# Kernel tuning notes

Hardware: AMD Instinct MI355X
Metric: run time of the kernel (lower is better)

## Reference

```python
import jax, jax.numpy as jnp
import numpy as np

B, NPG = 128, 512            # graphs, nodes per graph (batch is contiguous & uniform)
N = B * NPG                  # 65536 nodes
DEG = 8
E = N * DEG                  # 524288 edges
F_IN, NHID = 128, 64
H, C = 3, NHID               # GAT heads, out channels per head
HC = H * C                   # 192
NCLS = 10
RATIO = 0.5
NEG_SLOPE = 0.2


def setup_inputs() -> dict:
    key = jax.random.key(0)
    ks = jax.random.split(key, 24)
    x = jax.random.normal(ks[0], (N, F_IN), jnp.float32)
    # edges constrained within each graph (graphs are contiguous blocks of NPG nodes)
    offs = jnp.repeat(jnp.arange(B, dtype=jnp.int32) * NPG, NPG * DEG)
    src = jax.random.randint(ks[1], (E,), 0, NPG, dtype=jnp.int32) + offs
    dst = jax.random.randint(ks[2], (E,), 0, NPG, dtype=jnp.int32) + offs
    edge_index = jnp.stack([src, dst], axis=0)
    edge_attr = jax.random.normal(ks[3], (E, 2), jnp.float32)
    batch = jnp.repeat(jnp.arange(B, dtype=jnp.int32), NPG)

    def lin(k, o, i):
        return jax.random.normal(k, (o, i), jnp.float32) / np.float32(np.sqrt(i))

    return {
        "x": x, "edge_index": edge_index, "edge_attr": edge_attr, "batch": batch,
        # lin: num_features -> nhid//2
        "W_lin": lin(ks[4], NHID // 2, F_IN), "b_lin": jnp.zeros((NHID // 2,), jnp.float32),
        # GATConv(nhid//2 -> nhid, heads=3, edge_dim=2)
        "W_src": lin(ks[5], HC, NHID // 2),
        "att_src": jax.random.normal(ks[6], (H, C), jnp.float32) / np.float32(np.sqrt(C)),
        "att_dst": jax.random.normal(ks[7], (H, C), jnp.float32) / np.float32(np.sqrt(C)),
        "W_edge": lin(ks[8], HC, 2),
        "att_edge": jax.random.normal(ks[9], (H, C), jnp.float32) / np.float32(np.sqrt(C)),
        "b_gat": jnp.zeros((HC,), jnp.float32),
        # SAGPool score layer: GCNConv(nhid*3 -> 1)
        "W_gcn": lin(ks[10], 1, HC), "b_gcn": jnp.zeros((1,), jnp.float32),
        # classifier MLP
        "W1": lin(ks[11], NHID, 2 * HC), "b1": jnp.zeros((NHID,), jnp.float32),
        "W2": lin(ks[12], NHID // 2, NHID), "b2": jnp.zeros((NHID // 2,), jnp.float32),
        "W3": lin(ks[13], NCLS, NHID // 2), "b3": jnp.zeros((NCLS,), jnp.float32),
    }


def reference(x, edge_index, edge_attr, batch,
              W_lin, b_lin, W_src, att_src, att_dst, W_edge, att_edge, b_gat,
              W_gcn, b_gcn, W1, b1, W2, b2, W3, b3):
    src, dst = edge_index[0], edge_index[1]

    # ---- lin + ELU -------------------------------------------------------
    h = jax.nn.elu(x @ W_lin.T + b_lin)                       # [N, nhid//2]

    # ---- GATConv(heads=3, edge_dim=2), add_self_loops fill_value='mean' --
    loop = jnp.arange(N, dtype=src.dtype)
    cnt = jax.ops.segment_sum(jnp.ones((E,), h.dtype), dst, num_segments=N)
    loop_attr = jax.ops.segment_sum(edge_attr, dst, num_segments=N) / jnp.maximum(cnt, 1.0)[:, None]
    s_full = jnp.concatenate([src, loop])
    d_full = jnp.concatenate([dst, loop])
    ea_full = jnp.concatenate([edge_attr, loop_attr], axis=0)  # [E+N, 2]

    xp = (h @ W_src.T).reshape(N, H, C)                        # projected per-head feats
    a_src = (xp * att_src).sum(-1)                             # [N, H]
    a_dst = (xp * att_dst).sum(-1)                             # [N, H]
    ef = (ea_full @ W_edge.T).reshape(-1, H, C)
    a_edge = (ef * att_edge).sum(-1)                           # [E+N, H]

    alpha = jax.nn.leaky_relu(a_src[s_full] + a_dst[d_full] + a_edge, NEG_SLOPE)
    m = jax.ops.segment_max(alpha, d_full, num_segments=N)     # scatter-softmax over dst
    ealpha = jnp.exp(alpha - m[d_full])
    denom = jax.ops.segment_sum(ealpha, d_full, num_segments=N)
    alpha = ealpha / (denom[d_full] + 1e-16)                   # [E+N, H]

    out = jax.ops.segment_sum(alpha[:, :, None] * xp[s_full], d_full, num_segments=N)
    x1 = jax.nn.relu(out.reshape(N, HC) + b_gat)               # [N, 192]

    # ---- SAGPool: GCNConv score + per-graph top-k (mask form) ------------
    xw = x1 @ W_gcn.T                                          # [N, 1]
    deg = jax.ops.segment_sum(jnp.ones((E,), x1.dtype), dst, num_segments=N) + 1.0
    dinv = jax.lax.rsqrt(deg)
    agg = jax.ops.segment_sum((dinv[src] * dinv[dst])[:, None] * xw[src], dst, num_segments=N)
    score = (agg + (dinv ** 2)[:, None] * xw + b_gcn)[:, 0]    # [N]

    k = int(np.ceil(RATIO * NPG))                              # nodes kept per graph
    s2 = score.reshape(B, NPG)
    rank = jnp.argsort(jnp.argsort(-s2, axis=1), axis=1)
    mask = rank < k                                            # [B, NPG] top-k selection

    xs = (x1 * jnp.tanh(score)[:, None]).reshape(B, NPG, HC)
    gmp = jnp.max(jnp.where(mask[:, :, None], xs, -jnp.inf), axis=1)   # [B, 192]
    gap = jnp.sum(jnp.where(mask[:, :, None], xs, 0.0), axis=1) / k    # [B, 192]
    r = jnp.concatenate([gmp, gap], axis=1)                    # [B, 384]

    # ---- classifier MLP (dropout is identity in eval) ---------------------
    r = jax.nn.relu(r @ W1.T + b1)
    r = jax.nn.relu(r @ W2.T + b2)
    return jax.nn.log_softmax(r @ W3.T + b3, axis=-1)          # [B, num_classes]
```

## Files before the change

kernel.cpp:

```cpp
#include <hip/hip_runtime.h>
#include <hip/hip_bf16.h>
#include <math.h>

#define NN   65536
#define EE   524288
#define BB   128
#define NPGC 512
#define HCC  192
#define KSEL 256
#define NEG  0.2f
#define PSEG 16
#define SEGN (NPGC / PSEG)
#define MAXD 40
#define SLOTS ((size_t)NN * MAXD)
#define EPG   4096
#define HSTR  36

__device__ __forceinline__ int nodeblock_base(int bx) {
    int xcd = bx & 7, j = bx >> 3;
    int g = xcd + 8 * (j >> 1);
    return g * NPGC + (j & 1) * 256;
}

__global__ __launch_bounds__(192) void k_v(
    const float* __restrict__ W_src, const float* __restrict__ att_src,
    const float* __restrict__ att_dst, const float* __restrict__ W_edge,
    const float* __restrict__ att_edge, float* __restrict__ vbuf) {
    __shared__ float red[6];
    int t = threadIdx.x;
    if (t < 6) red[t] = 0.f;
    __syncthreads();
    {
        float ae = att_edge[t];
        int h = t >> 6;
        atomicAdd(&red[h],     W_edge[2 * t]     * ae);
        atomicAdd(&red[3 + h], W_edge[2 * t + 1] * ae);
    }
    if (t < 96) {
        int h = t >> 5, k = t & 31;
        float vs = 0.f, vd = 0.f;
        for (int c = 0; c < 64; ++c) {
            float w = W_src[(h * 64 + c) * 32 + k];
            vs += w * att_src[h * 64 + c];
            vd += w * att_dst[h * 64 + c];
        }
        vbuf[t] = vs;
        vbuf[96 + t] = vd;
    }
    __syncthreads();
    if (t < 6) vbuf[192 + t] = red[t];
}

__global__ __launch_bounds__(256) void k_feat(
    const float* __restrict__ x, const float* __restrict__ W_lin,
    const float* __restrict__ b_lin, const float* __restrict__ W_src,
    const float* __restrict__ vbuf,
    float* __restrict__ xp, float* __restrict__ ap_s, float* __restrict__ ap_d) {
    __shared__ float Wl[128 * HSTR];
    __shared__ float hs[128 * HSTR];
    __shared__ float vs_s[96], vd_s[96];
    int t = threadIdx.x;
    for (int i = t; i < 4096; i += 256) {
        int j = i >> 7, k = i & 127;
        Wl[k * HSTR + j] = W_lin[i];
    }
    if (t < 96) { vs_s[t] = vbuf[t]; vd_s[t] = vbuf[96 + t]; }
    __syncthreads();
    int bx = blockIdx.x;
    int xcd = bx & 7, j2 = bx >> 3;
    int g = xcd + 8 * (j2 >> 2);
    int nb = g * NPGC + (j2 & 3) * 128;
    int nl = t >> 1, hf = t & 1;
    int n = nb + nl;
    const float4* xr = (const float4*)(x + (size_t)n * 128);
    float acc[16];
#pragma unroll
    for (int j = 0; j < 16; ++j) acc[j] = b_lin[hf * 16 + j];
#pragma unroll 4
    for (int q = 0; q < 32; ++q) {
        float4 a = xr[q];
        const float* w = &Wl[(q * 4) * HSTR + hf * 16];
#pragma unroll
        for (int j = 0; j < 16; ++j) {
            acc[j] += a.x * w[j] + a.y * w[HSTR + j] +
                      a.z * w[2 * HSTR + j] + a.w * w[3 * HSTR + j];
        }
    }
#pragma unroll
    for (int j = 0; j < 16; ++j)
        acc[j] = acc[j] > 0.f ? acc[j] : expm1f(acc[j]);
#pragma unroll
    for (int head = 0; head < 3; ++head) {
        float s = 0.f, d = 0.f;
#pragma unroll
        for (int j = 0; j < 16; ++j) {
            s += acc[j] * vs_s[head * 32 + hf * 16 + j];
            d += acc[j] * vd_s[head * 32 + hf * 16 + j];
        }
        s += __shfl_xor(s, 1, 64);
        d += __shfl_xor(d, 1, 64);
        if (hf == 0) {
            ap_s[(size_t)head * NN + n] = s;
            ap_d[(size_t)head * NN + n] = d;
        }
    }
    float4* hw = (float4*)&hs[nl * HSTR + hf * 16];
#pragma unroll
    for (int q = 0; q < 4; ++q)
        hw[q] = make_float4(acc[4 * q], acc[4 * q + 1],
                            acc[4 * q + 2], acc[4 * q + 3]);
    __syncthreads();
    int lane = t & 63, wave = t >> 6;
    float wreg[96];
#pragma unroll
    for (int h = 0; h < 3; ++h) {
        const float4* wp = (const float4*)(W_src + (h * 64 + lane) * 32);
#pragma unroll
        for (int q = 0; q < 8; ++q) {
            float4 w = wp[q];
            wreg[h * 32 + 4 * q]     = w.x;
            wreg[h * 32 + 4 * q + 1] = w.y;
            wreg[h * 32 + 4 * q + 2] = w.z;
            wreg[h * 32 + 4 * q + 3] = w.w;
        }
    }
    int n0 = wave * 32;
    for (int nd = 0; nd < 32; ++nd) {
        int nl2 = n0 + nd;
        const float4* hr = (const float4*)&hs[nl2 * HSTR];
        float a0 = 0.f, a1 = 0.f, a2 = 0.f;
#pragma unroll
        for (int q = 0; q < 8; ++q) {
            float4 hv = hr[q];
            a0 += hv.x*wreg[4*q] + hv.y*wreg[4*q+1] + hv.z*wreg[4*q+2] + hv.w*wreg[4*q+3];
            a1 += hv.x*wreg[32+4*q] + hv.y*wreg[32+4*q+1] + hv.z*wreg[32+4*q+2] + hv.w*wreg[32+4*q+3];
            a2 += hv.x*wreg[64+4*q] + hv.y*wreg[64+4*q+1] + hv.z*wreg[64+4*q+2] + hv.w*wreg[64+4*q+3];
        }
        size_t nbase = (size_t)(nb + nl2) * HCC;
        xp[nbase + lane] = a0;
        xp[nbase + 64 + lane] = a1;
        xp[nbase + 128 + lane] = a2;
    }
}

__global__ __launch_bounds__(1024) void k_edges(
    const int* __restrict__ ei, const float* __restrict__ ea,
    const float* __restrict__ ap_s, const float* __restrict__ ap_d,
    const float* __restrict__ vbuf,
    int* __restrict__ fill, float4* __restrict__ slotA) {
    __shared__ int   s_pos[NPGC];
    __shared__ float s_la[NPGC * 2];
    __shared__ float s_as[NPGC * 3], s_ad[NPGC * 3];
    int b = blockIdx.x, t = threadIdx.x;
    int g = (b & 7) + 8 * (b >> 3);
    int nbase = g * NPGC;
    int ebase = g * EPG;
    if (t < NPGC) s_pos[t] = 0;
    s_la[t] = 0.f;
    for (int i = t; i < NPGC * 3; i += 1024) {
        int h = i >> 9, nl = i & (NPGC - 1);
        s_as[nl * 3 + h] = ap_s[(size_t)h * NN + nbase + nl];
        s_ad[nl * 3 + h] = ap_d[(size_t)h * NN + nbase + nl];
    }
    float ac[6];
#pragma unroll
    for (int h = 0; h < 6; ++h) ac[h] = vbuf[192 + h];
    int4  se  = ((const int4*)(ei + ebase))[t];
    int4  de  = ((const int4*)(ei + EE + ebase))[t];
    float4 a0 = ((const float4*)(ea + 2 * ebase))[2 * t];
    float4 a1 = ((const float4*)(ea + 2 * ebase))[2 * t + 1];
    __syncthreads();

    int   ss[4] = {se.x, se.y, se.z, se.w};
    int   dd[4] = {de.x, de.y, de.z, de.w};
    float e0v[4] = {a0.x, a0.z, a1.x, a1.z};
    float e1v[4] = {a0.y, a0.w, a1.y, a1.w};
#pragma unroll
    for (int k = 0; k < 4; ++k) {
        int s = ss[k], d = dd[k];
        int sl = s & (NPGC - 1), dl = d & (NPGC - 1);
        float e0 = e0v[k], e1 = e1v[k];
        atomicAdd(&s_la[2 * dl],     e0);
        atomicAdd(&s_la[2 * dl + 1], e1);
        float v[3];
#pragma unroll
        for (int h = 0; h < 3; ++h) {
            float a = s_as[sl * 3 + h] + s_ad[dl * 3 + h] +
                      e0 * ac[h] + e1 * ac[3 + h];
            v[h] = a >= 0.f ? a : NEG * a;
        }
        int pos = atomicAdd(&s_pos[dl], 1);
        if (pos < MAXD - 1)
            slotA[(size_t)(nbase + dl) * MAXD + 1 + pos] =
                make_float4(v[0], v[1], v[2], __int_as_float(s));
    }
    __syncthreads();
    if (t < NPGC) {
        int cnt = s_pos[t];
        int n = nbase + t;
        fill[n] = cnt;
        float inv = 1.f / fmaxf((float)cnt, 1.f);
        float l0 = s_la[2 * t] * inv, l1 = s_la[2 * t + 1] * inv;
        float v[3];
#pragma unroll
        for (int h = 0; h < 3; ++h) {
            float a = s_as[t * 3 + h] + s_ad[t * 3 + h] +
                      l0 * ac[h] + l1 * ac[3 + h];
            v[h] = a >= 0.f ? a : NEG * a;
        }
        slotA[(size_t)n * MAXD] = make_float4(v[0], v[1], v[2],
                                              __int_as_float(n));
    }
}

__global__ __launch_bounds__(256) void k_agg(
    const int* __restrict__ fill, const float4* __restrict__ slotA,
    const float* __restrict__ xp,
    const float* __restrict__ b_gat, const float* __restrict__ W_gcn,
    float* __restrict__ x1, float* __restrict__ xwd, float* __restrict__ dinv) {
    __shared__ float2 wsl[4][3][65];
    int wave = threadIdx.x >> 6, lane = threadIdx.x & 63;
    int b = blockIdx.x;
    int xcd = b & 7, j = b >> 3;
    int g = (j >> 7) * 8 + xcd;
    int n = g * NPGC + (j & 127) * 4 + wave;

    int ctrue = fill[n];
    int cnt = ctrue < (MAXD - 1) ? ctrue : (MAXD - 1);
    int tot = cnt + 1;

    if (lane < tot) {
        float4 pk = slotA[(size_t)n * MAXD + lane];
        wsl[wave][0][lane] = make_float2(__expf(pk.x), pk.w);
        wsl[wave][1][lane] = make_float2(__expf(pk.y), pk.w);
        wsl[wave][2][lane] = make_float2(__expf(pk.z), pk.w);
    }
    bool act = lane < 48;
    int head = act ? (lane >> 4) : 0;
    const float2* wp = &wsl[wave][head][0];
    const float4* xp4 = (const float4*)xp;
    float ax = 0.f, ay = 0.f, az = 0.f, aw = 0.f, den = 0.f;
    int s = 0;
    for (; s + 3 < tot; s += 4) {
        float2 wsA = wp[s],     wsB = wp[s + 1];
        float2 wsC = wp[s + 2], wsD = wp[s + 3];
        den += (wsA.x + wsB.x) + (wsC.x + wsD.x);
        if (act) {
            float4 vA = xp4[(size_t)__float_as_int(wsA.y) * 48 + lane];
            float4 vB = xp4[(size_t)__float_as_int(wsB.y) * 48 + lane];
            float4 vC = xp4[(size_t)__float_as_int(wsC.y) * 48 + lane];
            float4 vD = xp4[(size_t)__float_as_int(wsD.y) * 48 + lane];
            ax += wsA.x * vA.x + wsB.x * vB.x + wsC.x * vC.x + wsD.x * vD.x;
            ay += wsA.x * vA.y + wsB.x * vB.y + wsC.x * vC.y + wsD.x * vD.y;
            az += wsA.x * vA.z + wsB.x * vB.z + wsC.x * vC.z + wsD.x * vD.z;
            aw += wsA.x * vA.w + wsB.x * vB.w + wsC.x * vC.w + wsD.x * vD.w;
        }
    }
    for (; s < tot; ++s) {
        float2 wsA = wp[s];
        den += wsA.x;
        if (act) {
            float4 vA = xp4[(size_t)__float_as_int(wsA.y) * 48 + lane];
            ax += wsA.x * vA.x; ay += wsA.x * vA.y;
            az += wsA.x * vA.z; aw += wsA.x * vA.w;
        }
    }
    float p = 0.f;
    if (act) {
        float id = 1.f / (den + 1e-16f);
        float4 bg = ((const float4*)b_gat)[lane];
        float4 v;
        v.x = fmaxf(ax * id + bg.x, 0.f);
        v.y = fmaxf(ay * id + bg.y, 0.f);
        v.z = fmaxf(az * id + bg.z, 0.f);
        v.w = fmaxf(aw * id + bg.w, 0.f);
        ((float4*)x1)[(size_t)n * 48 + lane] = v;
        float4 wg = ((const float4*)W_gcn)[lane];
        p = v.x * wg.x + v.y * wg.y + v.z * wg.z + v.w * wg.w;
    }
#pragma unroll
    for (int msk = 32; msk > 0; msk >>= 1) p += __shfl_xor(p, msk, 64);
    if (lane == 0) {
        float dv = rsqrtf((float)ctrue + 1.f);
        xwd[n] = p * dv;
        dinv[n] = dv;
    }
}

__global__ __launch_bounds__(256) void k_score(
    const int* __restrict__ fill, const float4* __restrict__ slotA,
    const float* __restrict__ xwd, const float* __restrict__ dinv,
    const float* __restrict__ b_gcn, float* __restrict__ score) {
    int wave = threadIdx.x >> 6, lane = threadIdx.x & 63;
    int b = blockIdx.x;
    int xcd = b & 7, j = b >> 3;
    int g = (j >> 7) * 8 + xcd;
    int n = g * NPGC + (j & 127) * 4 + wave;

    int ctrue = fill[n];
    int cnt = ctrue < (MAXD - 1) ? ctrue : (MAXD - 1);
    float acc = 0.f;
    if (lane <= cnt) {
        int src = __float_as_int(
            ((const float*)slotA)[((size_t)n * MAXD + lane) * 4 + 3]);
        acc = xwd[src];
    }
#pragma unroll
    for (int msk = 32; msk > 0; msk >>= 1) acc += __shfl_xor(acc, msk, 64);
    if (lane == 0) score[n] = b_gcn[0] + dinv[n] * acc;
}

__global__ __launch_bounds__(192) void k_poolrank(
    const float* __restrict__ score, const float* __restrict__ x1,
    float* __restrict__ pmax, float* __restrict__ psum) {
    __shared__ float sc[NPGC];
    __shared__ float ts_s[SEGN];
    __shared__ int sel_s[SEGN];
    int b = blockIdx.x;
    int xcd = b & 7, gslot = (b >> 3) & 15, seg = b >> 7;
    int g = gslot * 8 + xcd;
    int t = threadIdx.x;
    int gbase = g * NPGC;
    for (int i = t; i < NPGC; i += 192) sc[i] = score[gbase + i];
    __syncthreads();
    if (t < SEGN) {
        int iloc = seg * SEGN + t;
        float si = sc[iloc];
        int rank = 0;
        for (int j = 0; j < NPGC; ++j) {
            float sj = sc[j];
            rank += (sj > si) || (sj == si && j < iloc);
        }
        sel_s[t] = (rank < KSEL) ? 1 : 0;
        ts_s[t] = tanhf(si);
    }
    __syncthreads();
    int nb = gbase + seg * SEGN;
    float mx = -1e30f, sm = 0.f;
    for (int i = 0; i < SEGN; ++i) {
        if (sel_s[i]) {
            float v = x1[(size_t)(nb + i) * HCC + t] * ts_s[i];
            mx = fmaxf(mx, v);
            sm += v;
        }
    }
    size_t pb = (size_t)(g * PSEG + seg) * HCC + t;
    pmax[pb] = mx;
    psum[pb] = sm;
}

__global__ __launch_bounds__(384) void k_mlp(
    const float* __restrict__ pmax, const float* __restrict__ psum,
    const float* __restrict__ W1, const float* __restrict__ b1,
    const float* __restrict__ W2, const float* __restrict__ b2,
    const float* __restrict__ W3, const float* __restrict__ b3,
    float* __restrict__ out) {
    __shared__ float rs[384], part[384], h1[64], h2[32], lg[10], mls;
    int g = blockIdx.x, t = threadIdx.x;
    if (t < HCC) {
        float mx = -1e30f, sm = 0.f;
#pragma unroll
        for (int s = 0; s < PSEG; ++s) {
            mx = fmaxf(mx, pmax[(size_t)(g * PSEG + s) * HCC + t]);
            sm += psum[(size_t)(g * PSEG + s) * HCC + t];
        }
        rs[t] = mx;
        rs[HCC + t] = sm * (1.f / (float)KSEL);
    }
    __syncthreads();
    {
        int o = t / 6, sl = t - o * 6;
        const float* wr = W1 + o * 384 + sl * 64;
        const float* rr = rs + sl * 64;
        float s = 0.f;
#pragma unroll 8
        for (int k = 0; k < 64; ++k) s += rr[k] * wr[k];
        part[t] = s;
    }
    __syncthreads();
    if (t < 64) {
        float s = b1[t];
#pragma unroll
        for (int j = 0; j < 6; ++j) s += part[t * 6 + j];
        h1[t] = fmaxf(s, 0.f);
    }
    __syncthreads();
    if (t < 256) {
        int o = t >> 3, sl = t & 7;
        const float* wr = W2 + o * 64 + sl * 8;
        const float* hr = h1 + sl * 8;
        float s = 0.f;
#pragma unroll
        for (int k = 0; k < 8; ++k) s += hr[k] * wr[k];
        part[t] = s;
    }
    __syncthreads();
    if (t < 32) {
        float s = b2[t];
#pragma unroll
        for (int j = 0; j < 8; ++j) s += part[t * 8 + j];
        h2[t] = fmaxf(s, 0.f);
    }
    __syncthreads();
    if (t < 10) {
        float s = b3[t];
        for (int k = 0; k < 32; ++k) s += h2[k] * W3[t * 32 + k];
        lg[t] = s;
    }
    __syncthreads();
    if (t == 0) {
        float mx = lg[0];
        for (int j = 1; j < 10; ++j) mx = fmaxf(mx, lg[j]);
        float se = 0.f;
        for (int j = 0; j < 10; ++j) se += expf(lg[j] - mx);
        mls = mx + logf(se);
    }
    __syncthreads();
    if (t < 10) out[g * 10 + t] = lg[t] - mls;
}

extern "C" void kernel_launch(void* const* d_in, const int* in_sizes, int n_in,
                              void* d_out, int out_size, void* d_ws, size_t ws_size,
                              hipStream_t stream) {
    const float* x        = (const float*)d_in[0];
    const int*   ei       = (const int*)d_in[1];
    const float* ea       = (const float*)d_in[2];
    const float* W_lin    = (const float*)d_in[4];
    const float* b_lin    = (const float*)d_in[5];
    const float* W_src    = (const float*)d_in[6];
    const float* att_src  = (const float*)d_in[7];
    const float* att_dst  = (const float*)d_in[8];
    const float* W_edge   = (const float*)d_in[9];
    const float* att_edge = (const float*)d_in[10];
    const float* b_gat    = (const float*)d_in[11];
    const float* W_gcn    = (const float*)d_in[12];
    const float* b_gcn    = (const float*)d_in[13];
    const float* W1 = (const float*)d_in[14]; const float* b1 = (const float*)d_in[15];
    const float* W2 = (const float*)d_in[16]; const float* b2 = (const float*)d_in[17];
    const float* W3 = (const float*)d_in[18]; const float* b3 = (const float*)d_in[19];
    float* out = (float*)d_out;

    char* ws = (char*)d_ws;
    size_t off = 0;
    auto alloc = [&](size_t bytes) {
        size_t r = off;
        off += (bytes + 255) & ~(size_t)255;
        return r;
    };
    float* xp      = (float*)(ws + alloc((size_t)NN * HCC * 4));
    float* x1      = (float*)(ws + alloc((size_t)NN * HCC * 4));
    int*   fill    = (int*)(ws + alloc((size_t)NN * 4));
    float* ap_s    = (float*)(ws + alloc((size_t)NN * 3 * 4));
    float* ap_d    = (float*)(ws + alloc((size_t)NN * 3 * 4));
    float4* slotA  = (float4*)(ws + alloc(SLOTS * 16));
    float* xwd     = (float*)(ws + alloc((size_t)NN * 4));
    float* dinv    = (float*)(ws + alloc((size_t)NN * 4));
    float* score   = (float*)(ws + alloc((size_t)NN * 4));
    float* vbuf    = (float*)(ws + alloc(256 * 4));
    float* pmax    = (float*)(ws + alloc((size_t)BB * PSEG * HCC * 4));
    float* psum    = (float*)(ws + alloc((size_t)BB * PSEG * HCC * 4));

    k_v<<<1, 192, 0, stream>>>(W_src, att_src, att_dst, W_edge, att_edge, vbuf);
    k_feat<<<512, 256, 0, stream>>>(x, W_lin, b_lin, W_src, vbuf,
                                    xp, ap_s, ap_d);
    k_edges<<<BB, 1024, 0, stream>>>(ei, ea, ap_s, ap_d, vbuf, fill, slotA);
    k_agg<<<NN / 4, 256, 0, stream>>>(fill, slotA, xp, b_gat, W_gcn,
                                      x1, xwd, dinv);
    k_score<<<NN / 4, 256, 0, stream>>>(fill, slotA, xwd, dinv, b_gcn, score);
    k_poolrank<<<BB * PSEG, 192, 0, stream>>>(score, x1, pmax, psum);
    k_mlp<<<BB, 384, 0, stream>>>(pmax, psum, W1, b1, W2, b2, W3, b3, out);
}
```

Baseline: 247.6 us.

## Register-tile k_feat linear layer with 4 nodes x 8 outputs per thread

```diff
diff --git a/kernel.cpp b/kernel.cpp
--- a/kernel.cpp
+++ b/kernel.cpp
@@ -16,12 +16,6 @@
 #define EPG   4096
 #define HSTR  36
 
-__device__ __forceinline__ int nodeblock_base(int bx) {
-    int xcd = bx & 7, j = bx >> 3;
-    int g = xcd + 8 * (j >> 1);
-    return g * NPGC + (j & 1) * 256;
-}
-
 __global__ __launch_bounds__(192) void k_v(
     const float* __restrict__ W_src, const float* __restrict__ att_src,
     const float* __restrict__ att_dst, const float* __restrict__ W_edge,
@@ -51,65 +45,113 @@
     if (t < 6) vbuf[192 + t] = red[t];
 }
 
-__global__ __launch_bounds__(256) void k_feat(
+__global__ __launch_bounds__(128) void k_feat(
     const float* __restrict__ x, const float* __restrict__ W_lin,
     const float* __restrict__ b_lin, const float* __restrict__ W_src,
     const float* __restrict__ vbuf,
     float* __restrict__ xp, float* __restrict__ ap_s, float* __restrict__ ap_d) {
     __shared__ float Wl[128 * HSTR];
     __shared__ float hs[128 * HSTR];
-    __shared__ float vs_s[96], vd_s[96];
+    __shared__ float apl[128][6];
     int t = threadIdx.x;
-    for (int i = t; i < 4096; i += 256) {
+    for (int i = t; i < 4096; i += 128) {
         int j = i >> 7, k = i & 127;
         Wl[k * HSTR + j] = W_lin[i];
     }
-    if (t < 96) { vs_s[t] = vbuf[t]; vd_s[t] = vbuf[96 + t]; }
-    __syncthreads();
     int bx = blockIdx.x;
     int xcd = bx & 7, j2 = bx >> 3;
     int g = xcd + 8 * (j2 >> 2);
     int nb = g * NPGC + (j2 & 3) * 128;
-    int nl = t >> 1, hf = t & 1;
-    int n = nb + nl;
-    const float4* xr = (const float4*)(x + (size_t)n * 128);
-    float acc[16];
-#pragma unroll
-    for (int j = 0; j < 16; ++j) acc[j] = b_lin[hf * 16 + j];
-#pragma unroll 4
+    int sl = t >> 5;
+    int nl0 = t & 31;
+    int j0 = (sl & 3) * 8;
+    float vS[24], vD[24];
+#pragma unroll
+    for (int h = 0; h < 3; ++h)
+#pragma unroll
+        for (int c = 0; c < 8; ++c) {
+            vS[h * 8 + c] = vbuf[h * 32 + j0 + c];
+            vD[h * 8 + c] = vbuf[96 + h * 32 + j0 + c];
+        }
+    float acc[4][8];
+#pragma unroll
+    for (int r = 0; r < 4; ++r)
+#pragma unroll
+        for (int c = 0; c < 8; ++c) acc[r][c] = b_lin[j0 + c];
+    const float4* xr0 = (const float4*)(x + (size_t)(nb + nl0) * 128);
+    const float4* xr1 = (const float4*)(x + (size_t)(nb + nl0 + 32) * 128);
+    const float4* xr2 = (const float4*)(x + (size_t)(nb + nl0 + 64) * 128);
+    const float4* xr3 = (const float4*)(x + (size_t)(nb + nl0 + 96) * 128);
+    __syncthreads();
+#pragma unroll 2
     for (int q = 0; q < 32; ++q) {
-        float4 a = xr[q];
-        const float* w = &Wl[(q * 4) * HSTR + hf * 16];
-#pragma unroll
-        for (int j = 0; j < 16; ++j) {
-            acc[j] += a.x * w[j] + a.y * w[HSTR + j] +
-                      a.z * w[2 * HSTR + j] + a.w * w[3 * HSTR + j];
-        }
-    }
-#pragma unroll
-    for (int j = 0; j < 16; ++j)
-        acc[j] = acc[j] > 0.f ? acc[j] : expm1f(acc[j]);
-#pragma unroll
-    for (int head = 0; head < 3; ++head) {
-        float s = 0.f, d = 0.f;
-#pragma unroll
-        for (int j = 0; j < 16; ++j) {
-            s += acc[j] * vs_s[head * 32 + hf * 16 + j];
-            d += acc[j] * vd_s[head * 32 + hf * 16 + j];
-        }
-        s += __shfl_xor(s, 1, 64);
-        d += __shfl_xor(d, 1, 64);
-        if (hf == 0) {
-            ap_s[(size_t)head * NN + n] = s;
-            ap_d[(size_t)head * NN + n] = d;
-        }
-    }
-    float4* hw = (float4*)&hs[nl * HSTR + hf * 16];
-#pragma unroll
-    for (int q = 0; q < 4; ++q)
-        hw[q] = make_float4(acc[4 * q], acc[4 * q + 1],
-                            acc[4 * q + 2], acc[4 * q + 3]);
-    __syncthreads();
+        float4 xa = xr0[q], xb = xr1[q], xc = xr2[q], xd = xr3[q];
+        float fa[4] = {xa.x, xa.y, xa.z, xa.w};
+        float fb[4] = {xb.x, xb.y, xb.z, xb.w};
+        float fc[4] = {xc.x, xc.y, xc.z, xc.w};
+        float fd[4] = {xd.x, xd.y, xd.z, xd.w};
+#pragma unroll
+        for (int kk = 0; kk < 4; ++kk) {
+            const float4* w4 = (const float4*)&Wl[(q * 4 + kk) * HSTR + j0];
+            float4 wA = w4[0], wB = w4[1];
+            float w8[8] = {wA.x, wA.y, wA.z, wA.w, wB.x, wB.y, wB.z, wB.w};
+#pragma unroll
+            for (int c = 0; c < 8; ++c) {
+                acc[0][c] += fa[kk] * w8[c];
+                acc[1][c] += fb[kk] * w8[c];
+                acc[2][c] += fc[kk] * w8[c];
+                acc[3][c] += fd[kk] * w8[c];
+            }
+        }
+    }
+    float ps[4][3], pd[4][3];
+#pragma unroll
+    for (int r = 0; r < 4; ++r) {
+#pragma unroll
+        for (int h = 0; h < 3; ++h) { ps[r][h] = 0.f; pd[r][h] = 0.f; }
+#pragma unroll
+        for (int c = 0; c < 8; ++c) {
+            float v = acc[r][c];
+            v = v > 0.f ? v : expm1f(v);
+            acc[r][c] = v;
+#pragma unroll
+            for (int h = 0; h < 3; ++h) {
+                ps[r][h] += v * vS[h * 8 + c];
+                pd[r][h] += v * vD[h * 8 + c];
+            }
+        }
+        float4* hw = (float4*)&hs[(nl0 + 32 * r) * HSTR + j0];
+        hw[0] = make_float4(acc[r][0], acc[r][1], acc[r][2], acc[r][3]);
+        hw[1] = make_float4(acc[r][4], acc[r][5], acc[r][6], acc[r][7]);
+    }
+#pragma unroll
+    for (int r = 0; r < 4; ++r)
+#pragma unroll
+        for (int h = 0; h < 3; ++h) {
+            ps[r][h] += __shfl_xor(ps[r][h], 32, 64);
+            pd[r][h] += __shfl_xor(pd[r][h], 32, 64);
+        }
+    if (t < 32) {
+#pragma unroll
+        for (int r = 0; r < 4; ++r)
+#pragma unroll
+            for (int h = 0; h < 3; ++h) {
+                apl[nl0 + 32 * r][h] = ps[r][h];
+                apl[nl0 + 32 * r][3 + h] = pd[r][h];
+            }
+    }
+    __syncthreads();
+    if (t >= 64 && t < 96) {
+#pragma unroll
+        for (int r = 0; r < 4; ++r) {
+            int n = nb + nl0 + 32 * r;
+#pragma unroll
+            for (int h = 0; h < 3; ++h) {
+                ap_s[(size_t)h * NN + n] = apl[nl0 + 32 * r][h] + ps[r][h];
+                ap_d[(size_t)h * NN + n] = apl[nl0 + 32 * r][3 + h] + pd[r][h];
+            }
+        }
+    }
     int lane = t & 63, wave = t >> 6;
     float wreg[96];
 #pragma unroll
@@ -124,8 +166,8 @@
             wreg[h * 32 + 4 * q + 3] = w.w;
         }
     }
-    int n0 = wave * 32;
-    for (int nd = 0; nd < 32; ++nd) {
+    int n0 = wave * 64;
+    for (int nd = 0; nd < 64; ++nd) {
         int nl2 = n0 + nd;
         const float4* hr = (const float4*)&hs[nl2 * HSTR];
         float a0 = 0.f, a1 = 0.f, a2 = 0.f;
@@ -461,7 +503,7 @@
     float* psum    = (float*)(ws + alloc((size_t)BB * PSEG * HCC * 4));
 
     k_v<<<1, 192, 0, stream>>>(W_src, att_src, att_dst, W_edge, att_edge, vbuf);
-    k_feat<<<512, 256, 0, stream>>>(x, W_lin, b_lin, W_src, vbuf,
+    k_feat<<<512, 128, 0, stream>>>(x, W_lin, b_lin, W_src, vbuf,
                                     xp, ap_s, ap_d);
     k_edges<<<BB, 1024, 0, stream>>>(ei, ea, ap_s, ap_d, vbuf, fill, slotA);
     k_agg<<<NN / 4, 256, 0, stream>>>(fill, slotA, xp, b_gat, W_gcn,
```

Result: slower. 259.5 us (+4.8%).
